# Kernel optimization log

Measured on AMD Instinct MI355X. Metric: run time of the kernel, lower is better.

Reference implementation:

```python
import jax, jax.numpy as jnp
import numpy as np

CODE_SIZE = 8
NUM_HEADS = 16
KC = 2 ** CODE_SIZE  # 256 codebook buckets


def setup_inputs() -> dict:
    key = jax.random.key(0)
    ks = jax.random.split(key, 6)
    B, Lq, Lk, C = 8, 2048, 4096, 1024
    q = jax.random.normal(ks[0], (B * Lq, C), jnp.float32)
    k = jax.random.normal(ks[1], (B * Lk, C), jnp.float32)
    v = jax.random.normal(ks[2], (B * Lk, C), jnp.float32)
    Wc = jax.random.normal(ks[3], (CODE_SIZE, C), jnp.float32) * (C ** -0.5)  # code_proj weight
    bc = jnp.zeros((CODE_SIZE,), jnp.float32)                                  # code_proj bias
    codebook = jax.random.normal(ks[4], (2 * CODE_SIZE, C), jnp.float32) * 0.02
    lengths = jnp.full((B,), Lk, jnp.int32)      # kv tokens per sample
    inv_lengths = jnp.full((B,), Lq, jnp.int32)  # q tokens per sample
    return dict(q=q, k=k, v=v, Wc=Wc, bc=bc, codebook=codebook,
                lengths=lengths, inv_lengths=inv_lengths)


def reference(q, k, v, Wc, bc, codebook, lengths, inv_lengths):
    C = q.shape[-1]
    d = C // NUM_HEADS
    scale = d ** -0.5
    B = lengths.shape[0]
    Lk = k.shape[0] // B  # equal per-sample kv lengths
    Lq = q.shape[0] // B  # equal per-sample q lengths

    # --- binary spherical quantization of k ---
    code = k @ Wc.T + bc
    code = code / jnp.linalg.norm(code, axis=-1, keepdims=True)
    # sign in {-1,+1}/sqrt(cs); affine *sqrt(cs)/2 + 0.5 -> bits in {0,1}
    bits = (code >= 0).astype(jnp.int32)                      # [B*Lk, cs]
    code_base = 2 ** jnp.arange(CODE_SIZE - 1, -1, -1)        # [cs]
    idxs = (bits * code_base).sum(-1)                         # [B*Lk] in [0, 256)

    # --- dense codebook keys for all 2^cs codes ---
    base_bits = (jnp.arange(KC)[:, None] // code_base) % 2    # [K, cs]
    base = jnp.concatenate([base_bits, 1 - base_bits], axis=-1).astype(codebook.dtype)  # [K, 2cs]
    cod_k = base @ codebook                                   # [K, C]

    # --- scatter-add v and counts into per-sample buckets ---
    b_idx = jnp.repeat(jnp.arange(B), Lk)                     # batch id per kv token
    flat = b_idx * KC + idxs                                  # [B*Lk]
    cod_v = jax.ops.segment_sum(v, flat, num_segments=B * KC).reshape(B, KC, C)
    counts = jax.ops.segment_sum(jnp.ones((B * Lk,), q.dtype), flat,
                                 num_segments=B * KC).reshape(B, KC)

    # --- bucketed attention with quotient normalization ---
    qh = q.reshape(B, Lq, NUM_HEADS, d)
    kh = cod_k.reshape(KC, NUM_HEADS, d)
    vh = cod_v.reshape(B, KC, NUM_HEADS, d)
    scores = scale * jnp.einsum('blhd,khd->blhk', qh, kh)     # [B,Lq,H,K]
    bias = jnp.where(counts > 0, 0.0, -jnp.inf)[:, None, None, :]  # mask empty buckets
    attn = jax.nn.softmax(scores + bias, axis=-1)
    num = jnp.einsum('blhk,bkhd->blhd', attn, vh)             # attn @ summed-v
    den = jnp.einsum('blhk,bk->blh', attn, counts)            # attn @ counts
    out = num / den[..., None]
    return out.reshape(B * Lq, C)
```

## Files before the change

kernel.cpp:

```cpp
#include <hip/hip_runtime.h>
#include <hip/hip_bf16.h>

constexpr int B  = 8;
constexpr int LQ = 2048;
constexpr int LK = 4096;
constexpr int C  = 1024;
constexpr int H  = 16;
constexpr int D  = 64;
constexpr int CS = 8;
constexpr int KC = 256;
constexpr float SCALE = 0.125f;

typedef __attribute__((ext_vector_type(8))) short short8;
typedef __attribute__((ext_vector_type(4))) float f32x4;

union FragU { unsigned u[4]; short8 s; float4 f; };

__device__ inline unsigned bfp(float a, float b) {
  __hip_bfloat16 x = __float2bfloat16(a), y = __float2bfloat16(b);
  unsigned short ux = *reinterpret_cast<unsigned short*>(&x);
  unsigned short uy = *reinterpret_cast<unsigned short*>(&y);
  return (unsigned)ux | ((unsigned)uy << 16);
}

__global__ __launch_bounds__(256) void k_codes(
    const float* __restrict__ kmat, const float* __restrict__ Wc,
    const float* __restrict__ bc, int* __restrict__ idx,
    float* __restrict__ counts)
{
  __shared__ float wS[CS * C];
  const int tid = threadIdx.x;
  {
    const float4* wsrc = (const float4*)Wc;
    float4* wdst = (float4*)wS;
#pragma unroll
    for (int i = 0; i < 8; ++i) wdst[tid + i * 256] = wsrc[tid + i * 256];
  }
  __syncthreads();

  const int wave = tid >> 6, lane = tid & 63;

  for (int i = 0; i < 8; ++i) {
    const int r = blockIdx.x * 32 + wave * 8 + i;
    const float4* krow = (const float4*)(kmat + (size_t)r * C);
    float acc[CS];
#pragma unroll
    for (int j = 0; j < CS; ++j) acc[j] = 0.f;
#pragma unroll
    for (int rep = 0; rep < 4; ++rep) {
      float4 kv = krow[rep * 64 + lane];
      const int dbase = (rep * 64 + lane) * 4;
#pragma unroll
      for (int j = 0; j < CS; ++j) {
        float4 wv = *(const float4*)&wS[j * C + dbase];
        acc[j] += kv.x * wv.x + kv.y * wv.y + kv.z * wv.z + kv.w * wv.w;
      }
    }
#pragma unroll
    for (int j = 0; j < CS; ++j) {
#pragma unroll
      for (int off = 32; off >= 1; off >>= 1)
        acc[j] += __shfl_xor(acc[j], off, 64);
    }
    if (lane == 0) {
      int ix = 0;
#pragma unroll
      for (int j = 0; j < CS; ++j) {
        float cj = acc[j] + bc[j];
        ix |= (cj >= 0.f ? 1 : 0) << (7 - j);
      }
      idx[r] = ix;
      const int bb = r >> 12;
      atomicAdd(&counts[bb * KC + ix], 1.0f);
    }
  }
}

__global__ __launch_bounds__(256) void k_offsets(
    const float* __restrict__ counts, int* __restrict__ offs,
    int* __restrict__ cursor)
{
  __shared__ int s[KC];
  const int t = threadIdx.x;
  for (int b = 0; b < B; ++b) {
    int myc = (int)counts[b * KC + t];
    s[t] = myc;
    __syncthreads();
#pragma unroll
    for (int off = 1; off < KC; off <<= 1) {
      int add = (t >= off) ? s[t - off] : 0;
      __syncthreads();
      s[t] += add;
      __syncthreads();
    }
    const int excl = s[t] - myc;
    offs[b * KC + t]   = b * LK + excl;
    cursor[b * KC + t] = b * LK + excl;
    __syncthreads();
  }
}

__global__ __launch_bounds__(256) void k_permute(
    const int* __restrict__ idx, int* __restrict__ cursor,
    int* __restrict__ perm)
{
  const int r = blockIdx.x * 256 + threadIdx.x;
  const int b = r >> 12;
  const int ix = idx[r];
  const int pos = atomicAdd(&cursor[b * KC + ix], 1);
  perm[pos] = r;
}

__global__ __launch_bounds__(256) void k_gather(
    const float* __restrict__ v, const int* __restrict__ perm,
    const int* __restrict__ offs, const float* __restrict__ counts,
    float* __restrict__ cod_v)
{
  __shared__ int permS[512];
  const int t = threadIdx.x;
  const int ix = blockIdx.x, b = blockIdx.y;
  const int start = offs[b * KC + ix];
  const int cnt = (int)counts[b * KC + ix];

  float4 acc = make_float4(0.f, 0.f, 0.f, 0.f);
  for (int base = 0; base < cnt; base += 512) {
    const int n = min(512, cnt - base);
    __syncthreads();
    for (int i = t; i < n; i += 256) permS[i] = perm[start + base + i];
    __syncthreads();
    int i = 0;
    for (; i + 4 <= n; i += 4) {
      const int r0 = permS[i], r1 = permS[i + 1];
      const int r2 = permS[i + 2], r3 = permS[i + 3];
      float4 a = *(const float4*)(v + (size_t)r0 * C + t * 4);
      float4 b4 = *(const float4*)(v + (size_t)r1 * C + t * 4);
      float4 c4 = *(const float4*)(v + (size_t)r2 * C + t * 4);
      float4 d4 = *(const float4*)(v + (size_t)r3 * C + t * 4);
      acc.x += a.x + b4.x + c4.x + d4.x;
      acc.y += a.y + b4.y + c4.y + d4.y;
      acc.z += a.z + b4.z + c4.z + d4.z;
      acc.w += a.w + b4.w + c4.w + d4.w;
    }
    for (; i < n; ++i) {
      const int r0 = permS[i];
      float4 a = *(const float4*)(v + (size_t)r0 * C + t * 4);
      acc.x += a.x; acc.y += a.y; acc.z += a.z; acc.w += a.w;
    }
  }
  *(float4*)(cod_v + (size_t)(b * KC + ix) * C + t * 4) = acc;
}

__global__ __launch_bounds__(256) void k_attn(
    const float* __restrict__ q, const float* __restrict__ cb,
    const float* __restrict__ cod_v, const float* __restrict__ counts,
    float* __restrict__ out)
{
  __shared__ __align__(16) char smem[59392];
  float4* VF = (float4*)smem;
  float4* QA = (float4*)(smem + 40960);
  float4* CBf = (float4*)(smem + 57344);
  float*  TS = (float*)(smem + 40960);

  const int tid = threadIdx.x;
  const int lane = tid & 63, wq = tid >> 6, quad = lane >> 4;
  const int h = blockIdx.y, b = blockIdx.z;
  const int q0 = blockIdx.x * 128;

#pragma unroll
  for (int it = 0; it < 8; ++it) {
    const int o = it * 4 + (tid >> 6);
    const int n = tid & 63;
    const float* src = cod_v + (size_t)(b * KC + o * 8) * C + h * D + n;
    float f[8];
#pragma unroll
    for (int r = 0; r < 8; ++r) f[r] = src[(size_t)r * C];
    FragU u;
    u.u[0] = bfp(f[0], f[1]); u.u[1] = bfp(f[2], f[3]);
    u.u[2] = bfp(f[4], f[5]); u.u[3] = bfp(f[6], f[7]);
    VF[((o >> 2) * 5 + (n >> 4)) * 64 + (o & 3) * 16 + (n & 15)] = u.f;
  }
  {
    float4 z4 = make_float4(0.f, 0.f, 0.f, 0.f);
    for (int i = tid; i < 512; i += 256) {
      const int qc = i >> 6, l = i & 63;
      if ((l & 15) != 0) VF[(qc * 5 + 4) * 64 + l] = z4;
    }
    if (tid < 32) {
      const int o = tid;
      const float* cs = counts + b * KC + o * 8;
      float f[8];
#pragma unroll
      for (int r = 0; r < 8; ++r) f[r] = cs[r];
      FragU u;
      u.u[0] = bfp(f[0], f[1]); u.u[1] = bfp(f[2], f[3]);
      u.u[2] = bfp(f[4], f[5]); u.u[3] = bfp(f[6], f[7]);
      VF[((o >> 2) * 5 + 4) * 64 + (o & 3) * 16] = u.f;
    }
  }
#pragma unroll
  for (int it = 0; it < 4; ++it) {
    const int od = tid & 7, m = it * 32 + (tid >> 3);
    const float* src = q + (size_t)(b * LQ + q0 + m) * C + h * D + od * 8;
    float4 f0 = *(const float4*)src, f1 = *(const float4*)(src + 4);
    FragU u;
    u.u[0] = bfp(f0.x * SCALE, f0.y * SCALE);
    u.u[1] = bfp(f0.z * SCALE, f0.w * SCALE);
    u.u[2] = bfp(f1.x * SCALE, f1.y * SCALE);
    u.u[3] = bfp(f1.z * SCALE, f1.w * SCALE);
    QA[((m >> 4) * 2 + (od >> 2)) * 64 + (od & 3) * 16 + (m & 15)] = u.f;
  }
  if (tid < 128) {
    const int od = tid & 7, j = tid >> 3;
    const float* src = cb + (size_t)j * C + h * D + od * 8;
    float4 f0 = *(const float4*)src, f1 = *(const float4*)(src + 4);
    FragU u;
    u.u[0] = bfp(f0.x, f0.y); u.u[1] = bfp(f0.z, f0.w);
    u.u[2] = bfp(f1.x, f1.y); u.u[3] = bfp(f1.z, f1.w);
    CBf[(od >> 2) * 64 + (od & 3) * 16 + j] = u.f;
  }
  __syncthreads();

  f32x4 tacc[2];
#pragma unroll
  for (int mt2 = 0; mt2 < 2; ++mt2) {
    const int mt = wq * 2 + mt2;
    FragU a0, a1, b0, b1;
    a0.f = QA[(mt * 2 + 0) * 64 + lane];
    a1.f = QA[(mt * 2 + 1) * 64 + lane];
    b0.f = CBf[0 * 64 + lane];
    b1.f = CBf[1 * 64 + lane];
    f32x4 z = {0.f, 0.f, 0.f, 0.f};
    z = __builtin_amdgcn_mfma_f32_16x16x32_bf16(a0.s, b0.s, z, 0, 0, 0);
    z = __builtin_amdgcn_mfma_f32_16x16x32_bf16(a1.s, b1.s, z, 0, 0, 0);
    tacc[mt2] = z;
  }
  __syncthreads();

#pragma unroll
  for (int mt2 = 0; mt2 < 2; ++mt2) {
    const int mt = wq * 2 + mt2;
#pragma unroll
    for (int r = 0; r < 4; ++r)
      TS[mt * 272 + (quad * 4 + r) * 17 + (lane & 15)] = tacc[mt2][r];
  }
  float t0[16], t1[16];
#pragma unroll
  for (int j = 0; j < 16; ++j) {
    t0[j] = TS[(wq * 2 + 0) * 272 + (lane & 15) * 17 + j];
    t1[j] = TS[(wq * 2 + 1) * 272 + (lane & 15) * 17 + j];
  }

  float sl0[8], sl1[8];
#pragma unroll
  for (int c = 0; c < 8; ++c) {
    sl0[c] = ((c & 4) ? t0[5] : t0[13]) + ((c & 2) ? t0[6] : t0[14]) +
             ((c & 1) ? t0[7] : t0[15]);
    sl1[c] = ((c & 4) ? t1[5] : t1[13]) + ((c & 2) ? t1[6] : t1[14]) +
             ((c & 1) ? t1[7] : t1[15]);
  }

  f32x4 acc[2][5];
#pragma unroll
  for (int i = 0; i < 2; ++i)
#pragma unroll
    for (int t_ = 0; t_ < 5; ++t_) acc[i][t_] = (f32x4){0.f, 0.f, 0.f, 0.f};

#pragma unroll
  for (int qc = 0; qc < 8; ++qc) {
    const int u = qc * 4 + quad;
    const float shi0 = ((u & 16) ? t0[0] : t0[8]) + ((u & 8) ? t0[1] : t0[9]) +
                       ((u & 4) ? t0[2] : t0[10]) + ((u & 2) ? t0[3] : t0[11]) +
                       ((u & 1) ? t0[4] : t0[12]);
    const float shi1 = ((u & 16) ? t1[0] : t1[8]) + ((u & 8) ? t1[1] : t1[9]) +
                       ((u & 4) ? t1[2] : t1[10]) + ((u & 2) ? t1[3] : t1[11]) +
                       ((u & 1) ? t1[4] : t1[12]);
    float p0[8], p1[8];
#pragma unroll
    for (int j = 0; j < 8; ++j) {
      p0[j] = __expf(shi0 + sl0[j]);
      p1[j] = __expf(shi1 + sl1[j]);
    }
    FragU a0, a1;
    a0.u[0] = bfp(p0[0], p0[1]); a0.u[1] = bfp(p0[2], p0[3]);
    a0.u[2] = bfp(p0[4], p0[5]); a0.u[3] = bfp(p0[6], p0[7]);
    a1.u[0] = bfp(p1[0], p1[1]); a1.u[1] = bfp(p1[2], p1[3]);
    a1.u[2] = bfp(p1[4], p1[5]); a1.u[3] = bfp(p1[6], p1[7]);
#pragma unroll
    for (int t_ = 0; t_ < 5; ++t_) {
      FragU bf_;
      bf_.f = VF[(qc * 5 + t_) * 64 + lane];
      acc[0][t_] = __builtin_amdgcn_mfma_f32_16x16x32_bf16(a0.s, bf_.s, acc[0][t_], 0, 0, 0);
      acc[1][t_] = __builtin_amdgcn_mfma_f32_16x16x32_bf16(a1.s, bf_.s, acc[1][t_], 0, 0, 0);
    }
  }

  const int srcl = lane & 48;
#pragma unroll
  for (int mt2 = 0; mt2 < 2; ++mt2) {
#pragma unroll
    for (int r = 0; r < 4; ++r) {
      const float den = __shfl(acc[mt2][4][r], srcl, 64);
      const float inv = 1.0f / den;
      const int row = q0 + wq * 32 + mt2 * 16 + quad * 4 + r;
      float* op = out + (size_t)(b * LQ + row) * C + h * D + (lane & 15);
#pragma unroll
      for (int t_ = 0; t_ < 4; ++t_) op[t_ * 16] = acc[mt2][t_][r] * inv;
    }
  }
}

extern "C" void kernel_launch(void* const* d_in, const int* in_sizes, int n_in,
                              void* d_out, int out_size, void* d_ws, size_t ws_size,
                              hipStream_t stream) {
  (void)in_sizes; (void)n_in; (void)out_size; (void)ws_size;
  const float* q  = (const float*)d_in[0];
  const float* k  = (const float*)d_in[1];
  const float* v  = (const float*)d_in[2];
  const float* Wc = (const float*)d_in[3];
  const float* bc = (const float*)d_in[4];
  const float* cb = (const float*)d_in[5];
  float* out = (float*)d_out;

  char* ws = (char*)d_ws;
  int*   idxp  = (int*)ws;
  float* cntp  = (float*)(ws + 0x20000);
  float* codvp = (float*)(ws + 0x28000);
  int*   offsp = (int*)(ws + 0x828000);
  int*   cursp = (int*)(ws + 0x82A000);
  int*   permp = (int*)(ws + 0x82C000);

  hipMemsetAsync(cntp, 0, B * KC * sizeof(float), stream);
  hipLaunchKernelGGL(k_codes, dim3(1024), dim3(256), 0, stream,
                     k, Wc, bc, idxp, cntp);
  hipLaunchKernelGGL(k_offsets, dim3(1), dim3(256), 0, stream,
                     cntp, offsp, cursp);
  hipLaunchKernelGGL(k_permute, dim3(B * LK / 256), dim3(256), 0, stream,
                     idxp, cursp, permp);
  hipLaunchKernelGGL(k_gather, dim3(KC, B), dim3(256), 0, stream,
                     v, permp, offsp, cntp, codvp);
  hipLaunchKernelGGL(k_attn, dim3(LQ / 128, H, B), dim3(256), 0, stream,
                     q, cb, codvp, cntp, out);
}
```

Before: 389.4 us.

## Pre-pack bf16 V fragments in gather, drop per-block V staging in attention

The gather kernel now writes bucket-summed V directly as bf16 in the MFMA B-fragment layout per (batch, head), and the offsets kernel (now one block per batch with a wave-shuffle scan) also emits the packed counts fragments. The attention kernel reads these fragments straight from global memory instead of re-converting fp32 cod_v into a 40KB LDS tile in every block, which shrinks LDS use and may raise occupancy. The softmax exponent is factored as exp(hi)*exp(lo), cutting expf calls per chunk, and bf16 pair conversion uses the packed intrinsic. The cost is uncoalesced 2-byte scattered stores in gather and more global or L2 fragment reads inside the MFMA loop.

```diff
diff --git a/kernel.cpp b/kernel.cpp
--- a/kernel.cpp
+++ b/kernel.cpp
@@ -17,10 +17,13 @@
 union FragU { unsigned u[4]; short8 s; float4 f; };
 
 __device__ inline unsigned bfp(float a, float b) {
-  __hip_bfloat16 x = __float2bfloat16(a), y = __float2bfloat16(b);
-  unsigned short ux = *reinterpret_cast<unsigned short*>(&x);
-  unsigned short uy = *reinterpret_cast<unsigned short*>(&y);
-  return (unsigned)ux | ((unsigned)uy << 16);
+  float2 f2; f2.x = a; f2.y = b;
+  __hip_bfloat162 h = __float22bfloat162_rn(f2);
+  return *reinterpret_cast<unsigned*>(&h);
+}
+__device__ inline unsigned short bf1(float a) {
+  __hip_bfloat16 h = __float2bfloat16(a);
+  return *reinterpret_cast<unsigned short*>(&h);
 }
 
 __global__ __launch_bounds__(256) void k_codes(
@@ -78,25 +81,39 @@
 
 __global__ __launch_bounds__(256) void k_offsets(
     const float* __restrict__ counts, int* __restrict__ offs,
-    int* __restrict__ cursor)
-{
-  __shared__ int s[KC];
-  const int t = threadIdx.x;
-  for (int b = 0; b < B; ++b) {
-    int myc = (int)counts[b * KC + t];
-    s[t] = myc;
-    __syncthreads();
-#pragma unroll
-    for (int off = 1; off < KC; off <<= 1) {
-      int add = (t >= off) ? s[t - off] : 0;
-      __syncthreads();
-      s[t] += add;
-      __syncthreads();
-    }
-    const int excl = s[t] - myc;
-    offs[b * KC + t]   = b * LK + excl;
-    cursor[b * KC + t] = b * LK + excl;
-    __syncthreads();
+    int* __restrict__ cursor, float4* __restrict__ vfc)
+{
+  __shared__ int wsum[4];
+  const int b = blockIdx.x, t = threadIdx.x;
+  const int lane = t & 63, w = t >> 6;
+  const int myc = (int)counts[b * KC + t];
+  int scan = myc;
+#pragma unroll
+  for (int off = 1; off < 64; off <<= 1) {
+    int u = __shfl_up(scan, off, 64);
+    if (lane >= off) scan += u;
+  }
+  if (lane == 63) wsum[w] = scan;
+  __syncthreads();
+  int base = 0;
+#pragma unroll
+  for (int i = 0; i < 4; ++i) base += (i < w) ? wsum[i] : 0;
+  const int excl = base + scan - myc;
+  offs[b * KC + t]   = b * LK + excl;
+  cursor[b * KC + t] = b * LK + excl;
+
+  for (int i = t; i < 512; i += 256) {
+    const int qc = i >> 6, ln = i & 63;
+    FragU u4;
+    if ((ln & 15) == 0) {
+      const int o = qc * 4 + (ln >> 4);
+      const float* cs = counts + b * KC + o * 8;
+      u4.u[0] = bfp(cs[0], cs[1]); u4.u[1] = bfp(cs[2], cs[3]);
+      u4.u[2] = bfp(cs[4], cs[5]); u4.u[3] = bfp(cs[6], cs[7]);
+    } else {
+      u4.u[0] = u4.u[1] = u4.u[2] = u4.u[3] = 0u;
+    }
+    vfc[b * 512 + i] = u4.f;
   }
 }
 
@@ -114,7 +131,7 @@
 __global__ __launch_bounds__(256) void k_gather(
     const float* __restrict__ v, const int* __restrict__ perm,
     const int* __restrict__ offs, const float* __restrict__ counts,
-    float* __restrict__ cod_v)
+    unsigned short* __restrict__ vbf)
 {
   __shared__ int permS[512];
   const int t = threadIdx.x;
@@ -147,56 +164,33 @@
       acc.x += a.x; acc.y += a.y; acc.z += a.z; acc.w += a.w;
     }
   }
-  *(float4*)(cod_v + (size_t)(b * KC + ix) * C + t * 4) = acc;
+
+  const int h = t >> 4;
+  const int n0 = (t & 15) * 4;
+  const int o = ix >> 3, r = ix & 7;
+  const int slot0 = ((o >> 2) * 4 + (n0 >> 4)) * 64 + (o & 3) * 16 + (n0 & 15);
+  unsigned short* dst = vbf + ((size_t)((b * 16 + h) * 2048 + slot0)) * 8 + r;
+  dst[0]  = bf1(acc.x);
+  dst[8]  = bf1(acc.y);
+  dst[16] = bf1(acc.z);
+  dst[24] = bf1(acc.w);
 }
 
 __global__ __launch_bounds__(256) void k_attn(
     const float* __restrict__ q, const float* __restrict__ cb,
-    const float* __restrict__ cod_v, const float* __restrict__ counts,
+    const float4* __restrict__ vfb, const float4* __restrict__ vfc,
     float* __restrict__ out)
 {
-  __shared__ __align__(16) char smem[59392];
-  float4* VF = (float4*)smem;
-  float4* QA = (float4*)(smem + 40960);
-  float4* CBf = (float4*)(smem + 57344);
-  float*  TS = (float*)(smem + 40960);
+  __shared__ __align__(16) char smem[18432];
+  float4* QA  = (float4*)smem;
+  float4* CBf = (float4*)(smem + 16384);
+  float*  TS  = (float*)smem;
 
   const int tid = threadIdx.x;
   const int lane = tid & 63, wq = tid >> 6, quad = lane >> 4;
   const int h = blockIdx.y, b = blockIdx.z;
   const int q0 = blockIdx.x * 128;
 
-#pragma unroll
-  for (int it = 0; it < 8; ++it) {
-    const int o = it * 4 + (tid >> 6);
-    const int n = tid & 63;
-    const float* src = cod_v + (size_t)(b * KC + o * 8) * C + h * D + n;
-    float f[8];
-#pragma unroll
-    for (int r = 0; r < 8; ++r) f[r] = src[(size_t)r * C];
-    FragU u;
-    u.u[0] = bfp(f[0], f[1]); u.u[1] = bfp(f[2], f[3]);
-    u.u[2] = bfp(f[4], f[5]); u.u[3] = bfp(f[6], f[7]);
-    VF[((o >> 2) * 5 + (n >> 4)) * 64 + (o & 3) * 16 + (n & 15)] = u.f;
-  }
-  {
-    float4 z4 = make_float4(0.f, 0.f, 0.f, 0.f);
-    for (int i = tid; i < 512; i += 256) {
-      const int qc = i >> 6, l = i & 63;
-      if ((l & 15) != 0) VF[(qc * 5 + 4) * 64 + l] = z4;
-    }
-    if (tid < 32) {
-      const int o = tid;
-      const float* cs = counts + b * KC + o * 8;
-      float f[8];
-#pragma unroll
-      for (int r = 0; r < 8; ++r) f[r] = cs[r];
-      FragU u;
-      u.u[0] = bfp(f[0], f[1]); u.u[1] = bfp(f[2], f[3]);
-      u.u[2] = bfp(f[4], f[5]); u.u[3] = bfp(f[6], f[7]);
-      VF[((o >> 2) * 5 + 4) * 64 + (o & 3) * 16] = u.f;
-    }
-  }
 #pragma unroll
   for (int it = 0; it < 4; ++it) {
     const int od = tid & 7, m = it * 32 + (tid >> 3);
@@ -250,13 +244,13 @@
     t1[j] = TS[(wq * 2 + 1) * 272 + (lane & 15) * 17 + j];
   }
 
-  float sl0[8], sl1[8];
+  float esl0[8], esl1[8];
 #pragma unroll
   for (int c = 0; c < 8; ++c) {
-    sl0[c] = ((c & 4) ? t0[5] : t0[13]) + ((c & 2) ? t0[6] : t0[14]) +
-             ((c & 1) ? t0[7] : t0[15]);
-    sl1[c] = ((c & 4) ? t1[5] : t1[13]) + ((c & 2) ? t1[6] : t1[14]) +
-             ((c & 1) ? t1[7] : t1[15]);
+    esl0[c] = __expf(((c & 4) ? t0[5] : t0[13]) + ((c & 2) ? t0[6] : t0[14]) +
+                     ((c & 1) ? t0[7] : t0[15]));
+    esl1[c] = __expf(((c & 4) ? t1[5] : t1[13]) + ((c & 2) ? t1[6] : t1[14]) +
+                     ((c & 1) ? t1[7] : t1[15]));
   }
 
   f32x4 acc[2][5];
@@ -265,33 +259,48 @@
 #pragma unroll
     for (int t_ = 0; t_ < 5; ++t_) acc[i][t_] = (f32x4){0.f, 0.f, 0.f, 0.f};
 
+  const float4* vb = vfb + (size_t)(b * 16 + h) * 2048 + lane;
+  const float4* vc = vfc + b * 512 + lane;
+
 #pragma unroll
   for (int qc = 0; qc < 8; ++qc) {
+    FragU bf0, bf1_, bf2, bf3, cf;
+    bf0.f = vb[(qc * 4 + 0) * 64];
+    bf1_.f = vb[(qc * 4 + 1) * 64];
+    bf2.f = vb[(qc * 4 + 2) * 64];
+    bf3.f = vb[(qc * 4 + 3) * 64];
+    cf.f  = vc[qc * 64];
+
     const int u = qc * 4 + quad;
-    const float shi0 = ((u & 16) ? t0[0] : t0[8]) + ((u & 8) ? t0[1] : t0[9]) +
-                       ((u & 4) ? t0[2] : t0[10]) + ((u & 2) ? t0[3] : t0[11]) +
-                       ((u & 1) ? t0[4] : t0[12]);
-    const float shi1 = ((u & 16) ? t1[0] : t1[8]) + ((u & 8) ? t1[1] : t1[9]) +
-                       ((u & 4) ? t1[2] : t1[10]) + ((u & 2) ? t1[3] : t1[11]) +
-                       ((u & 1) ? t1[4] : t1[12]);
-    float p0[8], p1[8];
-#pragma unroll
-    for (int j = 0; j < 8; ++j) {
-      p0[j] = __expf(shi0 + sl0[j]);
-      p1[j] = __expf(shi1 + sl1[j]);
-    }
+    const float eshi0 = __expf(
+        ((u & 16) ? t0[0] : t0[8]) + ((u & 8) ? t0[1] : t0[9]) +
+        ((u & 4) ? t0[2] : t0[10]) + ((u & 2) ? t0[3] : t0[11]) +
+        ((u & 1) ? t0[4] : t0[12]));
+    const float eshi1 = __expf(
+        ((u & 16) ? t1[0] : t1[8]) + ((u & 8) ? t1[1] : t1[9]) +
+        ((u & 4) ? t1[2] : t1[10]) + ((u & 2) ? t1[3] : t1[11]) +
+        ((u & 1) ? t1[4] : t1[12]));
+
     FragU a0, a1;
-    a0.u[0] = bfp(p0[0], p0[1]); a0.u[1] = bfp(p0[2], p0[3]);
-    a0.u[2] = bfp(p0[4], p0[5]); a0.u[3] = bfp(p0[6], p0[7]);
-    a1.u[0] = bfp(p1[0], p1[1]); a1.u[1] = bfp(p1[2], p1[3]);
-    a1.u[2] = bfp(p1[4], p1[5]); a1.u[3] = bfp(p1[6], p1[7]);
-#pragma unroll
-    for (int t_ = 0; t_ < 5; ++t_) {
-      FragU bf_;
-      bf_.f = VF[(qc * 5 + t_) * 64 + lane];
-      acc[0][t_] = __builtin_amdgcn_mfma_f32_16x16x32_bf16(a0.s, bf_.s, acc[0][t_], 0, 0, 0);
-      acc[1][t_] = __builtin_amdgcn_mfma_f32_16x16x32_bf16(a1.s, bf_.s, acc[1][t_], 0, 0, 0);
-    }
+    a0.u[0] = bfp(eshi0 * esl0[0], eshi0 * esl0[1]);
+    a0.u[1] = bfp(eshi0 * esl0[2], eshi0 * esl0[3]);
+    a0.u[2] = bfp(eshi0 * esl0[4], eshi0 * esl0[5]);
+    a0.u[3] = bfp(eshi0 * esl0[6], eshi0 * esl0[7]);
+    a1.u[0] = bfp(eshi1 * esl1[0], eshi1 * esl1[1]);
+    a1.u[1] = bfp(eshi1 * esl1[2], eshi1 * esl1[3]);
+    a1.u[2] = bfp(eshi1 * esl1[4], eshi1 * esl1[5]);
+    a1.u[3] = bfp(eshi1 * esl1[6], eshi1 * esl1[7]);
+
+    acc[0][0] = __builtin_amdgcn_mfma_f32_16x16x32_bf16(a0.s, bf0.s,  acc[0][0], 0, 0, 0);
+    acc[1][0] = __builtin_amdgcn_mfma_f32_16x16x32_bf16(a1.s, bf0.s,  acc[1][0], 0, 0, 0);
+    acc[0][1] = __builtin_amdgcn_mfma_f32_16x16x32_bf16(a0.s, bf1_.s, acc[0][1], 0, 0, 0);
+    acc[1][1] = __builtin_amdgcn_mfma_f32_16x16x32_bf16(a1.s, bf1_.s, acc[1][1], 0, 0, 0);
+    acc[0][2] = __builtin_amdgcn_mfma_f32_16x16x32_bf16(a0.s, bf2.s,  acc[0][2], 0, 0, 0);
+    acc[1][2] = __builtin_amdgcn_mfma_f32_16x16x32_bf16(a1.s, bf2.s,  acc[1][2], 0, 0, 0);
+    acc[0][3] = __builtin_amdgcn_mfma_f32_16x16x32_bf16(a0.s, bf3.s,  acc[0][3], 0, 0, 0);
+    acc[1][3] = __builtin_amdgcn_mfma_f32_16x16x32_bf16(a1.s, bf3.s,  acc[1][3], 0, 0, 0);
+    acc[0][4] = __builtin_amdgcn_mfma_f32_16x16x32_bf16(a0.s, cf.s,   acc[0][4], 0, 0, 0);
+    acc[1][4] = __builtin_amdgcn_mfma_f32_16x16x32_bf16(a1.s, cf.s,   acc[1][4], 0, 0, 0);
   }
 
   const int srcl = lane & 48;
@@ -322,22 +331,23 @@
   float* out = (float*)d_out;
 
   char* ws = (char*)d_ws;
-  int*   idxp  = (int*)ws;
-  float* cntp  = (float*)(ws + 0x20000);
-  float* codvp = (float*)(ws + 0x28000);
-  int*   offsp = (int*)(ws + 0x828000);
-  int*   cursp = (int*)(ws + 0x82A000);
-  int*   permp = (int*)(ws + 0x82C000);
+  int*    idxp = (int*)ws;
+  float*  cntp = (float*)(ws + 0x20000);
+  int*    offsp = (int*)(ws + 0x22000);
+  int*    cursp = (int*)(ws + 0x24000);
+  int*    permp = (int*)(ws + 0x26000);
+  float4* vfcp  = (float4*)(ws + 0x46000);
+  unsigned short* vbfp = (unsigned short*)(ws + 0x60000);
 
   hipMemsetAsync(cntp, 0, B * KC * sizeof(float), stream);
   hipLaunchKernelGGL(k_codes, dim3(1024), dim3(256), 0, stream,
                      k, Wc, bc, idxp, cntp);
-  hipLaunchKernelGGL(k_offsets, dim3(1), dim3(256), 0, stream,
-                     cntp, offsp, cursp);
+  hipLaunchKernelGGL(k_offsets, dim3(B), dim3(256), 0, stream,
+                     cntp, offsp, cursp, vfcp);
   hipLaunchKernelGGL(k_permute, dim3(B * LK / 256), dim3(256), 0, stream,
                      idxp, cursp, permp);
   hipLaunchKernelGGL(k_gather, dim3(KC, B), dim3(256), 0, stream,
-                     v, permp, offsp, cntp, codvp);
+                     v, permp, offsp, cntp, vbfp);
   hipLaunchKernelGGL(k_attn, dim3(LQ / 128, H, B), dim3(256), 0, stream,
-                     q, cb, codvp, cntp, out);
-}
+                     q, cb, (const float4*)vbfp, (const float4*)vfcp, out);
+}
```

New measurement: 378.6 us. -2.8%, faster.
